# Kernel optimization log

Hardware: AMD Instinct MI355X
Metric: run time of the kernel (lower is better)

Reference implementation:

```python
import jax, jax.numpy as jnp
import numpy as np

TOP_K = 2
NUM_EXPERTS = 8


def setup_inputs() -> dict:
    key = jax.random.key(0)
    ks = jax.random.split(key, 8)
    h, d, ds, E = 1024, 512, 1024, NUM_EXPERTS
    s = 1.0 / np.sqrt(h)
    return {
        "x": jax.random.normal(ks[0], (2, 2048, h), jnp.float32),
        "router": jax.random.normal(ks[1], (h, E), jnp.float32) * s,
        "experts_gate": jax.random.normal(ks[2], (E, h, d), jnp.float32) * s,
        "experts_up": jax.random.normal(ks[3], (E, h, d), jnp.float32) * s,
        "experts_down": jax.random.normal(ks[4], (E, d, h), jnp.float32) * (1.0 / np.sqrt(d)),
        "shared_gate": jax.random.normal(ks[5], (h, ds), jnp.float32) * s,
        "shared_up": jax.random.normal(ks[6], (h, ds), jnp.float32) * s,
        "shared_down": jax.random.normal(ks[7], (ds, h), jnp.float32) * (1.0 / np.sqrt(ds)),
    }


def reference(x, router, experts_gate, experts_up, experts_down,
              shared_gate, shared_up, shared_down):
    b, s, h = x.shape
    E = router.shape[1]
    # Shared expert path (SwiGLU)
    shared_act = jax.nn.silu(jnp.einsum('bsh,hd->bsd', x, shared_gate))
    shared_up_out = jnp.einsum('bsh,hd->bsd', x, shared_up)
    shared_out = jnp.einsum('bsd,dh->bsh', shared_act * shared_up_out, shared_down)
    # Router: softmax over experts, top-k selection
    router_probs = jax.nn.softmax(jnp.einsum('bsh,he->bse', x, router), axis=-1)
    topk_probs, topk_idx = jax.lax.top_k(router_probs, TOP_K)  # [b,s,k]
    # Dense per-token expert coefficient matrix: coef[t,e] = prob if expert e selected else 0
    coef = jnp.sum(jax.nn.one_hot(topk_idx, E, dtype=x.dtype) * topk_probs[..., None], axis=2)
    coef = coef.reshape(b * s, E)  # [T,E]
    x_flat = x.reshape(b * s, h)
    # Grouped expert SwiGLU (mathematically identical to gather->gemm->scatter_add;
    # unrouted token contributions are zeroed by coef)
    gate = jnp.einsum('th,ehd->etd', x_flat, experts_gate)
    up = jnp.einsum('th,ehd->etd', x_flat, experts_up)
    expert_out = jnp.einsum('etd,edh->eth', jax.nn.silu(gate) * up, experts_down)
    routed = jnp.einsum('eth,te->th', expert_out, coef)
    return routed.reshape(b, s, h) + shared_out
```

## Files before the change

kernel.cpp:

```cpp
#include <hip/hip_runtime.h>
#include <hip/hip_bf16.h>
#include <stdint.h>

typedef short bf16x8 __attribute__((ext_vector_type(8)));
typedef float f32x4 __attribute__((ext_vector_type(4)));
typedef unsigned short u16;

#define GLOAD16(gp, lp)                                                        \
  __builtin_amdgcn_global_load_lds(                                            \
      (const __attribute__((address_space(1))) void*)(gp),                     \
      (__attribute__((address_space(3))) void*)(lp), 16, 0, 0)

__device__ __forceinline__ u16 f2bf(float f) {
  uint32_t u = __builtin_bit_cast(uint32_t, f);
  u = (u + 0x7FFFu + ((u >> 16) & 1u)) >> 16;
  return (u16)u;
}
__device__ __forceinline__ float bf2f(u16 v) {
  return __builtin_bit_cast(float, (uint32_t)v << 16);
}

__device__ __forceinline__ int swzoff(int row, int u) {
  int p = row >> 1;
  int us = ((row & 1) * 4 + u) ^ (p & 7);
  return p * 128 + us * 16;
}

__global__ void mega(const float* __restrict__ x, const float* __restrict__ rw,
                     const float* __restrict__ eg, const float* __restrict__ eu,
                     const float* __restrict__ ed, const float* __restrict__ sg,
                     const float* __restrict__ su, const float* __restrict__ sd,
                     u16* __restrict__ Xb, u16* __restrict__ WpT,
                     u16* __restrict__ Wd2, u16* __restrict__ Wds,
                     float4* __restrict__ meta) {
  __shared__ float t[64][65];
  const int tid = threadIdx.x;
  const int b = blockIdx.x;
  if (b < 1280) {
    const float* src; int k0, h0;
    const bool is_e = b < 1024;
    if (is_e) { src = ed; k0 = (b >> 4) * 64;          h0 = (b & 15) * 64; }
    else      { src = sd; k0 = ((b - 1024) >> 4) * 64; h0 = (b & 15) * 64; }
#pragma unroll
    for (int p = 0; p < 4; ++p) {
      int r = p * 16 + (tid >> 4), c = (tid & 15) * 4;
      float4 v = *(const float4*)&src[(size_t)(k0 + r) * 1024 + h0 + c];
      t[r][c] = v.x; t[r][c + 1] = v.y; t[r][c + 2] = v.z; t[r][c + 3] = v.w;
    }
    __syncthreads();
#pragma unroll
    for (int p = 0; p < 4; ++p) {
      int hl = p * 16 + (tid >> 4), kl = (tid & 15) * 4;
      ushort4 o;
      o.x = f2bf(t[kl][hl]);     o.y = f2bf(t[kl + 1][hl]);
      o.z = f2bf(t[kl + 2][hl]); o.w = f2bf(t[kl + 3][hl]);
      if (is_e) {
        int kk = k0 + kl;
        int e = kk >> 9, dk = kk & 511;
        *(ushort4*)&Wd2[(size_t)e * 524288 + (size_t)(h0 + hl) * 512 + dk] = o;
      } else {
        *(ushort4*)&Wds[(size_t)(h0 + hl) * 1024 + k0 + kl] = o;
      }
    }
  } else if (b < 3840) {
    int bb = b - 1280;
    const float* src; int pbase, C, dt, ht;
    if (bb < 2048) {
      int slice = bb >> 7, r = bb & 127;
      int e = slice >> 1; int up = slice & 1;
      src = (up ? eu : eg) + (size_t)e * 524288;
      pbase = e * 1024 + up * 32; C = 512;
      dt = r >> 4; ht = r & 15;
    } else {
      int r = bb - 2048;
      int up = r >= 256; r &= 255;
      src = up ? su : sg; pbase = 8192 + up * 32; C = 1024;
      dt = r >> 4; ht = r & 15;
    }
    const int d0 = dt * 64, h0 = ht * 64;
#pragma unroll
    for (int p = 0; p < 4; ++p) {
      int hl = p * 16 + (tid >> 4), dl = (tid & 15) * 4;
      float4 v = *(const float4*)&src[(size_t)(h0 + hl) * C + d0 + dl];
      t[hl][dl] = v.x; t[hl][dl + 1] = v.y; t[hl][dl + 2] = v.z; t[hl][dl + 3] = v.w;
    }
    __syncthreads();
#pragma unroll
    for (int p = 0; p < 4; ++p) {
      int dl = p * 16 + (tid >> 4), hl = (tid & 15) * 4;
      int d = d0 + dl;
      int prow = pbase + ((d >> 5) << 6) + (d & 31);
      ushort4 o;
      o.x = f2bf(t[hl][dl]);     o.y = f2bf(t[hl + 1][dl]);
      o.z = f2bf(t[hl + 2][dl]); o.w = f2bf(t[hl + 3][dl]);
      *(ushort4*)&WpT[(size_t)prow * 1024 + h0 + hl] = o;
    }
  } else if (b < 4864) {
    const int l = tid & 63;
    const int tok = (b - 3840) * 4 + (tid >> 6);
    const float* xr = x + (size_t)tok * 1024;
    float acc[8];
#pragma unroll
    for (int e = 0; e < 8; ++e) acc[e] = 0.f;
    for (int it = 0; it < 16; ++it) {
      int h = it * 64 + l;
      float xv = xr[h];
      float4 r0 = *(const float4*)&rw[h * 8];
      float4 r1 = *(const float4*)&rw[h * 8 + 4];
      acc[0] += xv * r0.x; acc[1] += xv * r0.y; acc[2] += xv * r0.z; acc[3] += xv * r0.w;
      acc[4] += xv * r1.x; acc[5] += xv * r1.y; acc[6] += xv * r1.z; acc[7] += xv * r1.w;
    }
#pragma unroll
    for (int off = 32; off >= 1; off >>= 1) {
#pragma unroll
      for (int e = 0; e < 8; ++e) acc[e] += __shfl_xor(acc[e], off, 64);
    }
    if (l == 0) {
      float m = acc[0];
#pragma unroll
      for (int e = 1; e < 8; ++e) m = fmaxf(m, acc[e]);
      float p[8], s = 0.f;
#pragma unroll
      for (int e = 0; e < 8; ++e) { p[e] = expf(acc[e] - m); s += p[e]; }
      int i1 = 0;
#pragma unroll
      for (int e = 1; e < 8; ++e) if (p[e] > p[i1]) i1 = e;
      int i2 = (i1 == 0) ? 1 : 0;
#pragma unroll
      for (int e = 0; e < 8; ++e) if (e != i1 && p[e] > p[i2]) i2 = e;
      float inv = 1.f / s;
      meta[tok] = make_float4(__int_as_float(i1), __int_as_float(i2),
                              p[i1] * inv, p[i2] * inv);
    }
  } else {
    int i = (b - 4864) * 512 + tid;
#pragma unroll
    for (int k = 0; k < 2; ++k) {
      float4 v = ((const float4*)x)[i + k * 256];
      ushort4 o;
      o.x = f2bf(v.x); o.y = f2bf(v.y); o.z = f2bf(v.z); o.w = f2bf(v.w);
      ((ushort4*)Xb)[i + k * 256] = o;
    }
  }
}

__global__ __launch_bounds__(512) void assign_k(const float4* __restrict__ meta,
                                                int* __restrict__ counts_g,
                                                int* __restrict__ list_tok,
                                                int2* __restrict__ t2s) {
  __shared__ u16 sel[4096];
  __shared__ int cnt_s[8];
  const int tid = threadIdx.x;
  for (int i = tid; i < 4096; i += 512) {
    float4 m = meta[i];
    sel[i] = (u16)(__float_as_int(m.x) | (__float_as_int(m.y) << 8));
  }
  __syncthreads();

  const int E = tid >> 6;
  const int lane = tid & 63;
  const unsigned long long lt = (lane == 63) ? ~0ull >> 1 : ((1ull << lane) - 1ull);

  int total = 0;
#pragma unroll 8
  for (int it = 0; it < 64; ++it) {
    u16 s = sel[it * 64 + lane];
    bool any = ((s & 255) == E) || ((s >> 8) == E);
    total += __popcll(__ballot(any));
  }
  if (lane == 0) { cnt_s[E] = total; counts_g[E] = total; }
  __syncthreads();
  int base = 0;
#pragma unroll
  for (int e = 0; e < 8; ++e) base += (e < E) ? cnt_s[e] : 0;

  int running = base;
  for (int it = 0; it < 64; ++it) {
    int tok = it * 64 + lane;
    u16 s = sel[tok];
    bool s1 = ((s & 255) == E);
    bool s2 = ((s >> 8) == E);
    unsigned long long mask = __ballot(s1 || s2);
    int pos = running + __popcll(mask & lt);
    if (s1 || s2) {
      list_tok[pos] = tok;
      if (s1) t2s[tok].x = pos;
      else    t2s[tok].y = pos;
    }
    running += __popcll(mask);
  }
}

template <int MODE>
__global__ __launch_bounds__(512, 2) void moe_gemm(
    const u16* __restrict__ Xb, const u16* __restrict__ WpT,
    const u16* __restrict__ Wd2, const u16* __restrict__ Wds,
    u16* __restrict__ Hs, u16* __restrict__ Hcomp, u16* __restrict__ Pb,
    float* __restrict__ out,
    const int* __restrict__ counts, const int* __restrict__ list_tok) {
  constexpr int SLOT = (128 + 256) * 64;
  constexpr int BOFF = 128 * 64;
  __shared__ __align__(16) char lds[3 * SLOT];

  const int tid = threadIdx.x;
  const int l = tid & 63, l15 = l & 15, lg = l >> 4;
  const int wv = tid >> 6, wr = wv >> 2, wc = wv & 3;

  const int id = blockIdx.x;
  const bool routed = id < 288;
  int expert = 0, m0 = 0, n0 = 0, base = 0, count = 0, nt;

  if (routed) {
    int mtf = id >> 2; n0 = (id & 3) * 256;
    int acc_ = 0, bas = 0, found = 0;
#pragma unroll
    for (int e = 0; e < 8; ++e) {
      int c = counts[e];
      int nm = (c + 127) >> 7;
      if (!found && mtf < acc_ + nm) {
        expert = e; m0 = (mtf - acc_) * 128; base = bas; count = c; found = 1;
      }
      acc_ += nm; bas += c;
    }
    if (!found) return;
  } else {
    int sid = id - 288;
    int xcd = sid & 7, pos = sid >> 3;
    int mG = xcd >> 1, nG = xcd & 1;
    if (MODE == 0) {
      int mL = pos & 7, nL = pos >> 3;
      m0 = (mG * 8 + mL) * 128; n0 = (nG * 4 + nL) * 256;
    } else {
      int mL = pos & 7, nL = pos >> 3;
      m0 = (mG * 8 + mL) * 128; n0 = (nG * 2 + nL) * 256;
    }
  }
  nt = (MODE == 1 && routed) ? 16 : 32;

  const char* gA0; const char* gB[2]; int lA0, lB[2];
  {
    int L = tid * 16;
    int p = L >> 7, uph = (L >> 4) & 7;
    int usw = uph ^ (p & 7);
    int row = 2 * p + (usw >> 2), ulog = usw & 3;
    const u16* ap;
    if (MODE == 0) {
      if (routed) {
        int ar = min(m0 + row, count - 1);
        ap = Xb + (size_t)list_tok[base + ar] * 1024;
      } else ap = Xb + (size_t)(m0 + row) * 1024;
    } else {
      if (routed) ap = Hcomp + (size_t)(base + min(m0 + row, count - 1)) * 512;
      else        ap = Hs + (size_t)(m0 + row) * 1024;
    }
    gA0 = (const char*)ap + ulog * 16;
    lA0 = L;
  }
#pragma unroll
  for (int j = 0; j < 2; ++j) {
    int L = (j * 512 + tid) * 16;
    int p = L >> 7, uph = (L >> 4) & 7;
    int usw = uph ^ (p & 7);
    int row = 2 * p + (usw >> 2), ulog = usw & 3;
    const u16* bp;
    if (MODE == 0) {
      int rbase = routed ? expert * 1024 : 8192;
      bp = WpT + (size_t)(rbase + n0 + row) * 1024;
    } else {
      if (routed) bp = Wd2 + (size_t)expert * 524288 + (size_t)(n0 + row) * 512;
      else        bp = Wds + (size_t)(n0 + row) * 1024;
    }
    gB[j] = (const char*)bp + ulog * 16;
    lB[j] = L;
  }

  int offA[4], offB[4];
#pragma unroll
  for (int m = 0; m < 4; ++m) offA[m] = swzoff(wr * 64 + m * 16 + l15, lg);
#pragma unroll
  for (int n = 0; n < 4; ++n) offB[n] = BOFF + swzoff(wc * 64 + n * 16 + l15, lg);

  f32x4 acc[4][4];
#pragma unroll
  for (int m = 0; m < 4; ++m)
#pragma unroll
    for (int n = 0; n < 4; ++n) acc[m][n] = {0.f, 0.f, 0.f, 0.f};

#define STAGE(T)                                                               \
  {                                                                            \
    char* sb_ = lds + (((T) % 3) * SLOT);                                      \
    const int tb_ = (T) * 64;                                                  \
    GLOAD16(gA0 + tb_, sb_ + lA0);                                             \
    GLOAD16(gB[0] + tb_, sb_ + BOFF + lB[0]);                                  \
    GLOAD16(gB[1] + tb_, sb_ + BOFF + lB[1]);                                  \
  }

  STAGE(0); STAGE(1);

  for (int t = 0; t < nt; ++t) {
    if (t + 1 < nt) {
      asm volatile("s_waitcnt vmcnt(3)" ::: "memory");
    } else {
      asm volatile("s_waitcnt vmcnt(0)" ::: "memory");
    }
    __builtin_amdgcn_s_barrier();
    asm volatile("" ::: "memory");
    char* sb = lds + ((t % 3) * SLOT);
    bf16x8 af[4], bfr[4];
#pragma unroll
    for (int m = 0; m < 4; ++m) af[m] = *(const bf16x8*)(sb + offA[m]);
#pragma unroll
    for (int n = 0; n < 4; ++n) bfr[n] = *(const bf16x8*)(sb + offB[n]);
    if (t + 2 < nt) STAGE(t + 2);
    __builtin_amdgcn_s_setprio(1);
#pragma unroll
    for (int m = 0; m < 4; ++m)
#pragma unroll
      for (int n = 0; n < 4; ++n)
        acc[m][n] = __builtin_amdgcn_mfma_f32_16x16x32_bf16(af[m], bfr[n], acc[m][n], 0, 0, 0);
    __builtin_amdgcn_s_setprio(0);
    asm volatile("" ::: "memory");
  }
#undef STAGE

  const int rbl = wr * 64 + lg * 4;
  const int cnt_lim = routed ? count : (1 << 30);
  if constexpr (MODE == 0) {
    u16* dst = routed ? Hcomp : Hs;
    const int ldH = routed ? 512 : 1024;
    const int rowbase = routed ? (base + m0) : m0;
    const int cD0 = (n0 + wc * 64) >> 1;
#pragma unroll
    for (int m = 0; m < 4; ++m)
#pragma unroll
      for (int q = 0; q < 2; ++q) {
        int cD = cD0 + q * 16 + l15;
#pragma unroll
        for (int j = 0; j < 4; ++j) {
          int mrow = rbl + m * 16 + j;
          if (m0 + mrow < cnt_lim) {
            float g = acc[m][q][j];
            float u = acc[m][q + 2][j];
            dst[(size_t)(rowbase + mrow) * ldH + cD] =
                f2bf(g / (1.f + __expf(-g)) * u);
          }
        }
      }
  } else {
    const int cb = n0 + wc * 64;
#pragma unroll
    for (int m = 0; m < 4; ++m)
#pragma unroll
      for (int n = 0; n < 4; ++n)
#pragma unroll
        for (int j = 0; j < 4; ++j) {
          int mrow = rbl + m * 16 + j;
          if (m0 + mrow < cnt_lim) {
            int col = cb + n * 16 + l15;
            if (routed)
              Pb[(size_t)(base + m0 + mrow) * 1024 + col] = f2bf(acc[m][n][j]);
            else
              out[(size_t)(m0 + mrow) * 1024 + col] = acc[m][n][j];
          }
        }
  }
}

__global__ void reduce_k(const float4* __restrict__ meta, const int2* __restrict__ t2s,
                         const u16* __restrict__ Pb, float* __restrict__ out) {
  const int t = blockIdx.x;
  const int c = threadIdx.x * 4;
  float4 m = meta[t];
  int2 s = t2s[t];
  float p1 = m.z, p2 = m.w;
  ushort4 a = *(const ushort4*)&Pb[(size_t)s.x * 1024 + c];
  ushort4 bb = *(const ushort4*)&Pb[(size_t)s.y * 1024 + c];
  float4 o = *(float4*)&out[(size_t)t * 1024 + c];
  o.x += p1 * bf2f(a.x) + p2 * bf2f(bb.x);
  o.y += p1 * bf2f(a.y) + p2 * bf2f(bb.y);
  o.z += p1 * bf2f(a.z) + p2 * bf2f(bb.z);
  o.w += p1 * bf2f(a.w) + p2 * bf2f(bb.w);
  *(float4*)&out[(size_t)t * 1024 + c] = o;
}

extern "C" void kernel_launch(void* const* d_in, const int* in_sizes, int n_in,
                              void* d_out, int out_size, void* d_ws, size_t ws_size,
                              hipStream_t stream) {
  const float* x  = (const float*)d_in[0];
  const float* rw = (const float*)d_in[1];
  const float* eg = (const float*)d_in[2];
  const float* eu = (const float*)d_in[3];
  const float* ed = (const float*)d_in[4];
  const float* sg = (const float*)d_in[5];
  const float* su = (const float*)d_in[6];
  const float* sd = (const float*)d_in[7];
  float* out = (float*)d_out;

  char* ws = (char*)d_ws;
  u16*    Xb    = (u16*)(ws);
  u16*    WpT   = (u16*)(ws + 8388608);
  u16*    Wd2   = (u16*)(ws + 29360128);
  u16*    Wds   = (u16*)(ws + 37748736);
  u16*    Hs    = (u16*)(ws + 39845888);
  u16*    Hcomp = (u16*)(ws + 48234496);
  u16*    Pb    = (u16*)(ws + 56623104);
  float4* meta  = (float4*)(ws + 73400320);
  int2*   t2s   = (int2*)(ws + 73465856);
  int*    counts= (int*)(ws + 73498624);
  int*    list_tok = (int*)(ws + 73498688);

  mega<<<6912, 256, 0, stream>>>(x, rw, eg, eu, ed, sg, su, sd,
                                 Xb, WpT, Wd2, Wds, meta);
  assign_k<<<1, 512, 0, stream>>>(meta, counts, list_tok, t2s);

  moe_gemm<0><<<544, 512, 0, stream>>>(Xb, WpT, Wd2, Wds, Hs, Hcomp, Pb, out,
                                       counts, list_tok);
  moe_gemm<1><<<416, 512, 0, stream>>>(Xb, WpT, Wd2, Wds, Hs, Hcomp, Pb, out,
                                       counts, list_tok);

  reduce_k<<<4096, 256, 0, stream>>>(meta, t2s, Pb, out);
}
```

Baseline: 128.6 us.

## Split-K the shared-expert down projection into two bf16 partials

The shared-expert down GEMM in the second grouped GEMM launch is split along K into two halves. This doubles its block count (416 to 544 blocks) and matches its per-block K length to the routed tiles. Each half writes a bf16 partial into workspace that reuses the no-longer-needed WpT region, and the final reduce kernel sums both partials with the weighted routed outputs, so it no longer reads out. The aim is better load balance and occupancy in the down-projection launch. The cost is extra partial-buffer traffic and bf16 rounding of the shared output.

```diff
diff --git a/kernel.cpp b/kernel.cpp
--- a/kernel.cpp
+++ b/kernel.cpp
@@ -196,7 +196,7 @@
     const u16* __restrict__ Xb, const u16* __restrict__ WpT,
     const u16* __restrict__ Wd2, const u16* __restrict__ Wds,
     u16* __restrict__ Hs, u16* __restrict__ Hcomp, u16* __restrict__ Pb,
-    float* __restrict__ out,
+    u16* __restrict__ Ps0, u16* __restrict__ Ps1,
     const int* __restrict__ counts, const int* __restrict__ list_tok) {
   constexpr int SLOT = (128 + 256) * 64;
   constexpr int BOFF = 128 * 64;
@@ -208,7 +208,7 @@
 
   const int id = blockIdx.x;
   const bool routed = id < 288;
-  int expert = 0, m0 = 0, n0 = 0, base = 0, count = 0, nt;
+  int expert = 0, m0 = 0, n0 = 0, base = 0, count = 0, nt, split = 0, kb = 0;
 
   if (routed) {
     int mtf = id >> 2; n0 = (id & 3) * 256;
@@ -231,11 +231,14 @@
       int mL = pos & 7, nL = pos >> 3;
       m0 = (mG * 8 + mL) * 128; n0 = (nG * 4 + nL) * 256;
     } else {
-      int mL = pos & 7, nL = pos >> 3;
+      split = pos & 1;
+      int q = pos >> 1;
+      int mL = q & 7, nL = q >> 3;
       m0 = (mG * 8 + mL) * 128; n0 = (nG * 2 + nL) * 256;
-    }
-  }
-  nt = (MODE == 1 && routed) ? 16 : 32;
+      kb = split * 512;
+    }
+  }
+  nt = (MODE == 1) ? 16 : 32;
 
   const char* gA0; const char* gB[2]; int lA0, lB[2];
   {
@@ -251,7 +254,7 @@
       } else ap = Xb + (size_t)(m0 + row) * 1024;
     } else {
       if (routed) ap = Hcomp + (size_t)(base + min(m0 + row, count - 1)) * 512;
-      else        ap = Hs + (size_t)(m0 + row) * 1024;
+      else        ap = Hs + (size_t)(m0 + row) * 1024 + kb;
     }
     gA0 = (const char*)ap + ulog * 16;
     lA0 = L;
@@ -268,7 +271,7 @@
       bp = WpT + (size_t)(rbase + n0 + row) * 1024;
     } else {
       if (routed) bp = Wd2 + (size_t)expert * 524288 + (size_t)(n0 + row) * 512;
-      else        bp = Wds + (size_t)(n0 + row) * 1024;
+      else        bp = Wds + (size_t)(n0 + row) * 1024 + kb;
     }
     gB[j] = (const char*)bp + ulog * 16;
     lB[j] = L;
@@ -348,6 +351,7 @@
       }
   } else {
     const int cb = n0 + wc * 64;
+    u16* dstS = split ? Ps1 : Ps0;
 #pragma unroll
     for (int m = 0; m < 4; ++m)
 #pragma unroll
@@ -360,26 +364,29 @@
             if (routed)
               Pb[(size_t)(base + m0 + mrow) * 1024 + col] = f2bf(acc[m][n][j]);
             else
-              out[(size_t)(m0 + mrow) * 1024 + col] = acc[m][n][j];
+              dstS[(size_t)(m0 + mrow) * 1024 + col] = f2bf(acc[m][n][j]);
           }
         }
   }
 }
 
 __global__ void reduce_k(const float4* __restrict__ meta, const int2* __restrict__ t2s,
-                         const u16* __restrict__ Pb, float* __restrict__ out) {
+                         const u16* __restrict__ Pb, const u16* __restrict__ Ps0,
+                         const u16* __restrict__ Ps1, float* __restrict__ out) {
   const int t = blockIdx.x;
   const int c = threadIdx.x * 4;
   float4 m = meta[t];
   int2 s = t2s[t];
   float p1 = m.z, p2 = m.w;
-  ushort4 a = *(const ushort4*)&Pb[(size_t)s.x * 1024 + c];
+  ushort4 a  = *(const ushort4*)&Pb[(size_t)s.x * 1024 + c];
   ushort4 bb = *(const ushort4*)&Pb[(size_t)s.y * 1024 + c];
-  float4 o = *(float4*)&out[(size_t)t * 1024 + c];
-  o.x += p1 * bf2f(a.x) + p2 * bf2f(bb.x);
-  o.y += p1 * bf2f(a.y) + p2 * bf2f(bb.y);
-  o.z += p1 * bf2f(a.z) + p2 * bf2f(bb.z);
-  o.w += p1 * bf2f(a.w) + p2 * bf2f(bb.w);
+  ushort4 u0 = *(const ushort4*)&Ps0[(size_t)t * 1024 + c];
+  ushort4 u1 = *(const ushort4*)&Ps1[(size_t)t * 1024 + c];
+  float4 o;
+  o.x = bf2f(u0.x) + bf2f(u1.x) + p1 * bf2f(a.x) + p2 * bf2f(bb.x);
+  o.y = bf2f(u0.y) + bf2f(u1.y) + p1 * bf2f(a.y) + p2 * bf2f(bb.y);
+  o.z = bf2f(u0.z) + bf2f(u1.z) + p1 * bf2f(a.z) + p2 * bf2f(bb.z);
+  o.w = bf2f(u0.w) + bf2f(u1.w) + p1 * bf2f(a.w) + p2 * bf2f(bb.w);
   *(float4*)&out[(size_t)t * 1024 + c] = o;
 }
 
@@ -399,6 +406,8 @@
   char* ws = (char*)d_ws;
   u16*    Xb    = (u16*)(ws);
   u16*    WpT   = (u16*)(ws + 8388608);
+  u16*    Ps0   = (u16*)(ws + 8388608);
+  u16*    Ps1   = (u16*)(ws + 16777216);
   u16*    Wd2   = (u16*)(ws + 29360128);
   u16*    Wds   = (u16*)(ws + 37748736);
   u16*    Hs    = (u16*)(ws + 39845888);
@@ -413,10 +422,10 @@
                                  Xb, WpT, Wd2, Wds, meta);
   assign_k<<<1, 512, 0, stream>>>(meta, counts, list_tok, t2s);
 
-  moe_gemm<0><<<544, 512, 0, stream>>>(Xb, WpT, Wd2, Wds, Hs, Hcomp, Pb, out,
-                                       counts, list_tok);
-  moe_gemm<1><<<416, 512, 0, stream>>>(Xb, WpT, Wd2, Wds, Hs, Hcomp, Pb, out,
-                                       counts, list_tok);
-
-  reduce_k<<<4096, 256, 0, stream>>>(meta, t2s, Pb, out);
-}
+  moe_gemm<0><<<544, 512, 0, stream>>>(Xb, WpT, Wd2, Wds, Hs, Hcomp, Pb,
+                                       Ps0, Ps1, counts, list_tok);
+  moe_gemm<1><<<544, 512, 0, stream>>>(Xb, WpT, Wd2, Wds, Hs, Hcomp, Pb,
+                                       Ps0, Ps1, counts, list_tok);
+
+  reduce_k<<<4096, 256, 0, stream>>>(meta, t2s, Pb, Ps0, Ps1, out);
+}
```

Measured after the change: 125.9 us, median of 2. -2.1%, faster.
